# Optimization experiments

Hardware: AMD Instinct MI355X
Metric: run time of the kernel (lower is better)

## Reference

```python
import jax, jax.numpy as jnp
import numpy as np

HIDDEN = 2048
INTER = 1408
NUM_EXPERTS = 8
TOP_K = 2
BATCH, SEQ = 2, 1024


def setup_inputs() -> dict:
    key = jax.random.key(0)
    ks = jax.random.split(key, 8)
    s = 0.02
    return {
        "x": jax.random.normal(ks[0], (BATCH, SEQ, HIDDEN), dtype=jnp.float32),
        "router_w": jax.random.normal(ks[1], (NUM_EXPERTS, HIDDEN), dtype=jnp.float32) * s,
        "gate_w": jax.random.normal(ks[2], (NUM_EXPERTS, INTER, HIDDEN), dtype=jnp.float32) * s,
        "up_w": jax.random.normal(ks[3], (NUM_EXPERTS, INTER, HIDDEN), dtype=jnp.float32) * s,
        "down_w": jax.random.normal(ks[4], (NUM_EXPERTS, HIDDEN, INTER), dtype=jnp.float32) * s,
        "shared_gate_w": jax.random.normal(ks[5], (INTER, HIDDEN), dtype=jnp.float32) * s,
        "shared_up_w": jax.random.normal(ks[6], (INTER, HIDDEN), dtype=jnp.float32) * s,
        "shared_down_w": jax.random.normal(ks[7], (HIDDEN, INTER), dtype=jnp.float32) * s,
    }


def reference(x, router_w, gate_w, up_w, down_w,
              shared_gate_w, shared_up_w, shared_down_w):
    B, S, H = x.shape
    T = B * S
    E = router_w.shape[0]
    xf = x.reshape(T, H)

    # Router: softmax over experts, top-k selection, renormalized weights
    logits = xf @ router_w.T                       # [T, E]
    probs = jax.nn.softmax(logits, axis=-1)
    topw, topi = jax.lax.top_k(probs, TOP_K)       # [T, K]
    topw = topw / jnp.sum(topw, axis=-1, keepdims=True)

    # Combine weight per (token, expert): scatter-add of top-k weights
    comb = jnp.zeros((T, E), dtype=xf.dtype).at[
        jnp.arange(T)[:, None], topi].add(topw)    # [T, E]

    # All-expert SwiGLU (grouped GEMM form of masked gather/MLP/scatter)
    g = jnp.einsum('th,eih->tei', xf, gate_w)      # [T, E, I]
    u = jnp.einsum('th,eih->tei', xf, up_w)
    hmid = jax.nn.silu(g) * u
    eo = jnp.einsum('tei,ehi->teh', hmid, down_w)  # [T, E, H]
    out = jnp.einsum('te,teh->th', comb, eo)       # weighted combine

    # Shared expert applied to every token
    sh = (jax.nn.silu(xf @ shared_gate_w.T) * (xf @ shared_up_w.T)) @ shared_down_w.T
    out = out + sh
    return out.reshape(B, S, H)
```

## Files before the change

### kernel.cpp

```cpp
#include <hip/hip_runtime.h>
#include <cstdint>
#include <cstddef>

#define T_TOK 2048
#define HID   2048
#define INTER 1408
#define NEXP  8
#define NPAIR 6144
#define SLICE 2883584
#define BKS   32

typedef __bf16 bf16x8 __attribute__((ext_vector_type(8)));
typedef float  floatx4 __attribute__((ext_vector_type(4)));

static const size_t XB_OFF   = 0;
static const size_t HM_OFF   = XB_OFF + (size_t)T_TOK * HID * 2;
static const size_t GB_OFF   = HM_OFF + (size_t)NPAIR * INTER * 2;
static const size_t UB_OFF   = GB_OFF + (size_t)9 * SLICE * 2;
static const size_t DB_OFF   = UB_OFF + (size_t)9 * SLICE * 2;
static const size_t TOK_OFF  = DB_OFF + (size_t)9 * SLICE * 2;
static const size_t WGT_OFF  = TOK_OFF + (size_t)NPAIR * 4;
static const size_t TE_OFF   = WGT_OFF + (size_t)NPAIR * 4;
static const size_t TW_OFF   = TE_OFF + (size_t)T_TOK * 2 * 4;
static const size_t CTRL_OFF = TW_OFF + (size_t)T_TOK * 2 * 4;

static __device__ __forceinline__ unsigned short f2bf(float f) {
    unsigned u = __float_as_uint(f);
    u += 0x7fffu + ((u >> 16) & 1u);
    return (unsigned short)(u >> 16);
}
static __device__ __forceinline__ unsigned pk2(float a, float b) {
    return (unsigned)f2bf(a) | ((unsigned)f2bf(b) << 16);
}
static __device__ __forceinline__ void g2l16(const void* g, void* l) {
    __builtin_amdgcn_global_load_lds(
        (const __attribute__((address_space(1))) unsigned int*)g,
        (__attribute__((address_space(3))) unsigned int*)l, 16, 0, 0);
}

__global__ __launch_bounds__(256) void k_cvt_x(const float* __restrict__ x,
                                               unsigned short* __restrict__ xb) {
    int gid = blockIdx.x * 256 + threadIdx.x;
    const float4* src = (const float4*)x;
    float4 a = src[gid * 2], b = src[gid * 2 + 1];
    uint4 o;
    o.x = pk2(a.x, a.y); o.y = pk2(a.z, a.w);
    o.z = pk2(b.x, b.y); o.w = pk2(b.z, b.w);
    ((uint4*)xb)[gid] = o;
}

__global__ __launch_bounds__(256) void k_cvt_w(const float* __restrict__ g,
                                               const float* __restrict__ u,
                                               const float* __restrict__ d,
                                               const float* __restrict__ sg,
                                               const float* __restrict__ su,
                                               const float* __restrict__ sd,
                                               unsigned short* __restrict__ gb,
                                               unsigned short* __restrict__ ub,
                                               unsigned short* __restrict__ db) {
    int sl = blockIdx.z;
    const float* src;
    unsigned short* dst;
    if (blockIdx.y == 0) {
        src = (sl < 8) ? g + (size_t)sl * SLICE : sg;
        dst = gb + (size_t)sl * SLICE;
    } else if (blockIdx.y == 1) {
        src = (sl < 8) ? u + (size_t)sl * SLICE : su;
        dst = ub + (size_t)sl * SLICE;
    } else {
        src = (sl < 8) ? d + (size_t)sl * SLICE : sd;
        dst = db + (size_t)sl * SLICE;
    }
    int gid = blockIdx.x * 256 + threadIdx.x;
    const float4* s4 = (const float4*)src;
    float4 a = s4[gid * 2], b = s4[gid * 2 + 1];
    uint4 o;
    o.x = pk2(a.x, a.y); o.y = pk2(a.z, a.w);
    o.z = pk2(b.x, b.y); o.w = pk2(b.z, b.w);
    ((uint4*)dst)[gid] = o;
}

__global__ __launch_bounds__(256) void k_router(const float* __restrict__ x,
                                                const float* __restrict__ rw,
                                                int* __restrict__ te, float* __restrict__ tw,
                                                int* __restrict__ counts) {
    int wave = threadIdx.x >> 6, lane = threadIdx.x & 63;
    int t = blockIdx.x * 4 + wave;
    const float* xp = x + (size_t)t * HID;

    float acc[8];
#pragma unroll
    for (int e = 0; e < 8; ++e) acc[e] = 0.f;
    for (int i = lane; i < HID; i += 64) {
        float xv = xp[i];
#pragma unroll
        for (int e = 0; e < 8; ++e) acc[e] = fmaf(xv, rw[e * HID + i], acc[e]);
    }
#pragma unroll
    for (int e = 0; e < 8; ++e) {
        float v = acc[e];
        for (int s = 32; s; s >>= 1) v += __shfl_xor(v, s, 64);
        acc[e] = v;
    }
    float mx = acc[0];
#pragma unroll
    for (int e = 1; e < 8; ++e) mx = fmaxf(mx, acc[e]);
    float p[8];
#pragma unroll
    for (int e = 0; e < 8; ++e) p[e] = __expf(acc[e] - mx);
    int i1 = 0; float v1 = p[0];
#pragma unroll
    for (int e = 1; e < 8; ++e) if (p[e] > v1) { v1 = p[e]; i1 = e; }
    int i2 = -1; float v2 = -1.f;
#pragma unroll
    for (int e = 0; e < 8; ++e) if (e != i1 && p[e] > v2) { v2 = p[e]; i2 = e; }
    float inv = 1.f / (v1 + v2);
    if (lane == 0) {
        te[2 * t] = i1;     tw[2 * t] = v1 * inv;
        te[2 * t + 1] = i2; tw[2 * t + 1] = v2 * inv;
        atomicAdd(&counts[i1], 1);
        atomicAdd(&counts[i2], 1);
    }
}

__global__ void k_offsets(int* __restrict__ ctrl) {
    if (threadIdx.x == 0) {
        int s = 0;
        for (int e = 0; e < 8; ++e) { ctrl[16 + e] = s; s += ctrl[e]; }
        ctrl[16 + 8] = s;
        ctrl[8] = T_TOK;
    }
}

__global__ __launch_bounds__(256) void k_scatter(const int* __restrict__ te,
                                                 const float* __restrict__ tw,
                                                 const int* __restrict__ offsets,
                                                 int* __restrict__ fill,
                                                 int* __restrict__ tok, float* __restrict__ wgt) {
    int t = blockIdx.x * 256 + threadIdx.x;
    if (t >= T_TOK) return;
#pragma unroll
    for (int k = 0; k < 2; ++k) {
        int e = te[2 * t + k];
        int slot = atomicAdd(&fill[e], 1);
        int pp = offsets[e] + slot;
        tok[pp] = t; wgt[pp] = tw[2 * t + k];
    }
    tok[2 * T_TOK + t] = t; wgt[2 * T_TOK + t] = 1.0f;
}

__global__ __launch_bounds__(256) void k_gemm1(const unsigned short* __restrict__ xb,
                                               const unsigned short* __restrict__ gwb,
                                               const unsigned short* __restrict__ uwb,
                                               const int* __restrict__ tok,
                                               const int* __restrict__ ctrl,
                                               unsigned short* __restrict__ hmid) {
    int e = blockIdx.z;
    int cnt = ctrl[e];
    int m0 = blockIdx.y * 128;
    if (m0 >= cnt) return;
    int off = ctrl[16 + e];
    int i0 = blockIdx.x * 64;
    const unsigned short* gw = gwb + (size_t)e * SLICE;
    const unsigned short* uw = uwb + (size_t)e * SLICE;

    __shared__ __align__(16) unsigned short As[128 * BKS];
    __shared__ __align__(16) unsigned short Bg[64 * BKS];
    __shared__ __align__(16) unsigned short Bu[64 * BKS];

    int tid = threadIdx.x;
    int lane = tid & 63, wave = tid >> 6;
    int lr = lane >> 2, lc = (lane & 3) * 8;

    int r0 = m0 + wave * 32 + lr;
    int ap0 = off + r0;       if (ap0 > NPAIR - 1) ap0 = NPAIR - 1;
    int ap1 = off + r0 + 16;  if (ap1 > NPAIR - 1) ap1 = NPAIR - 1;
    const unsigned short* a0 = xb + (size_t)tok[ap0] * HID + lc;
    const unsigned short* a1 = xb + (size_t)tok[ap1] * HID + lc;
    const unsigned short* bg = gw + (size_t)(i0 + wave * 16 + lr) * HID + lc;
    const unsigned short* bu = uw + (size_t)(i0 + wave * 16 + lr) * HID + lc;

    unsigned short* lA0 = &As[(wave * 32) * BKS];
    unsigned short* lA1 = &As[(wave * 32 + 16) * BKS];
    unsigned short* lBg = &Bg[(wave * 16) * BKS];
    unsigned short* lBu = &Bu[(wave * 16) * BKS];

    floatx4 accg[2][4], accu[2][4];
#pragma unroll
    for (int mi = 0; mi < 2; ++mi)
#pragma unroll
        for (int ni = 0; ni < 4; ++ni) {
            accg[mi][ni] = (floatx4){0.f, 0.f, 0.f, 0.f};
            accu[mi][ni] = (floatx4){0.f, 0.f, 0.f, 0.f};
        }

    int wm = wave * 32;
    int mrow = lane & 15, kq = (lane >> 4) * 8;

    for (int kt = 0; kt < HID / BKS; ++kt) {
        int k0 = kt * BKS;
        g2l16(a0 + k0, lA0);
        g2l16(a1 + k0, lA1);
        g2l16(bg + k0, lBg);
        g2l16(bu + k0, lBu);
        __syncthreads();

        bf16x8 af[2];
#pragma unroll
        for (int mi = 0; mi < 2; ++mi)
            af[mi] = *(const bf16x8*)&As[(wm + mi * 16 + mrow) * BKS + kq];
#pragma unroll
        for (int ni = 0; ni < 4; ++ni) {
            bf16x8 bgv = *(const bf16x8*)&Bg[(ni * 16 + mrow) * BKS + kq];
            bf16x8 buv = *(const bf16x8*)&Bu[(ni * 16 + mrow) * BKS + kq];
#pragma unroll
            for (int mi = 0; mi < 2; ++mi) {
                accg[mi][ni] = __builtin_amdgcn_mfma_f32_16x16x32_bf16(af[mi], bgv, accg[mi][ni], 0, 0, 0);
                accu[mi][ni] = __builtin_amdgcn_mfma_f32_16x16x32_bf16(af[mi], buv, accu[mi][ni], 0, 0, 0);
            }
        }
        __syncthreads();
    }

    int quad = lane >> 4, col = lane & 15;
#pragma unroll
    for (int mi = 0; mi < 2; ++mi)
#pragma unroll
        for (int ni = 0; ni < 4; ++ni)
#pragma unroll
            for (int r = 0; r < 4; ++r) {
                int row = m0 + wm + mi * 16 + quad * 4 + r;
                if (row < cnt) {
                    float g = accg[mi][ni][r], u = accu[mi][ni][r];
                    float s = g / (1.f + __expf(-g));
                    hmid[(size_t)(off + row) * INTER + i0 + ni * 16 + col] = f2bf(s * u);
                }
            }
}

__global__ __launch_bounds__(256) void k_gemm2(const unsigned short* __restrict__ hmid,
                                               const unsigned short* __restrict__ dwb,
                                               const int* __restrict__ tok,
                                               const float* __restrict__ wgt,
                                               const int* __restrict__ ctrl,
                                               float* __restrict__ out) {
    int e = blockIdx.z;
    int cnt = ctrl[e];
    int m0 = blockIdx.y * 128;
    if (m0 >= cnt) return;
    int off = ctrl[16 + e];
    int n0 = blockIdx.x * 64;
    const unsigned short* dw = dwb + (size_t)e * SLICE;

    __shared__ __align__(16) unsigned short As[128 * BKS];
    __shared__ __align__(16) unsigned short Bd[64 * BKS];

    int tid = threadIdx.x;
    int lane = tid & 63, wave = tid >> 6;
    int lr = lane >> 2, lc = (lane & 3) * 8;

    int r0 = m0 + wave * 32 + lr;
    int ap0 = off + r0;       if (ap0 > NPAIR - 1) ap0 = NPAIR - 1;
    int ap1 = off + r0 + 16;  if (ap1 > NPAIR - 1) ap1 = NPAIR - 1;
    const unsigned short* a0 = hmid + (size_t)ap0 * INTER + lc;
    const unsigned short* a1 = hmid + (size_t)ap1 * INTER + lc;
    const unsigned short* bd = dw + (size_t)(n0 + wave * 16 + lr) * INTER + lc;

    unsigned short* lA0 = &As[(wave * 32) * BKS];
    unsigned short* lA1 = &As[(wave * 32 + 16) * BKS];
    unsigned short* lBd = &Bd[(wave * 16) * BKS];

    floatx4 acc[2][4];
#pragma unroll
    for (int mi = 0; mi < 2; ++mi)
#pragma unroll
        for (int ni = 0; ni < 4; ++ni) acc[mi][ni] = (floatx4){0.f, 0.f, 0.f, 0.f};

    int wm = wave * 32;
    int mrow = lane & 15, kq = (lane >> 4) * 8;

    for (int kt = 0; kt < INTER / BKS; ++kt) {
        int k0 = kt * BKS;
        g2l16(a0 + k0, lA0);
        g2l16(a1 + k0, lA1);
        g2l16(bd + k0, lBd);
        __syncthreads();

        bf16x8 af[2];
#pragma unroll
        for (int mi = 0; mi < 2; ++mi)
            af[mi] = *(const bf16x8*)&As[(wm + mi * 16 + mrow) * BKS + kq];
#pragma unroll
        for (int ni = 0; ni < 4; ++ni) {
            bf16x8 bv = *(const bf16x8*)&Bd[(ni * 16 + mrow) * BKS + kq];
#pragma unroll
            for (int mi = 0; mi < 2; ++mi)
                acc[mi][ni] = __builtin_amdgcn_mfma_f32_16x16x32_bf16(af[mi], bv, acc[mi][ni], 0, 0, 0);
        }
        __syncthreads();
    }

    int quad = lane >> 4, col = lane & 15;
#pragma unroll
    for (int mi = 0; mi < 2; ++mi)
#pragma unroll
        for (int r = 0; r < 4; ++r) {
            int row = m0 + wm + mi * 16 + quad * 4 + r;
            if (row < cnt) {
                int p = off + row;
                int t = tok[p];
                float w = wgt[p];
#pragma unroll
                for (int ni = 0; ni < 4; ++ni)
                    atomicAdd(&out[(size_t)t * HID + n0 + ni * 16 + col], w * acc[mi][ni][r]);
            }
        }
}

extern "C" void kernel_launch(void* const* d_in, const int* in_sizes, int n_in,
                              void* d_out, int out_size, void* d_ws, size_t ws_size,
                              hipStream_t stream) {
    const float* x        = (const float*)d_in[0];
    const float* router_w = (const float*)d_in[1];
    const float* gate_w   = (const float*)d_in[2];
    const float* up_w     = (const float*)d_in[3];
    const float* down_w   = (const float*)d_in[4];
    const float* sgate    = (const float*)d_in[5];
    const float* sup      = (const float*)d_in[6];
    const float* sdown    = (const float*)d_in[7];
    float* out = (float*)d_out;

    char* ws = (char*)d_ws;
    unsigned short* xb   = (unsigned short*)(ws + XB_OFF);
    unsigned short* hmid = (unsigned short*)(ws + HM_OFF);
    unsigned short* gwb  = (unsigned short*)(ws + GB_OFF);
    unsigned short* uwb  = (unsigned short*)(ws + UB_OFF);
    unsigned short* dwb  = (unsigned short*)(ws + DB_OFF);
    int*   tok  = (int*)(ws + TOK_OFF);
    float* wgt  = (float*)(ws + WGT_OFF);
    int*   te   = (int*)(ws + TE_OFF);
    float* tw   = (float*)(ws + TW_OFF);
    int*   ctrl = (int*)(ws + CTRL_OFF);

    hipMemsetAsync(ctrl, 0, 48 * sizeof(int), stream);
    hipMemsetAsync(out, 0, (size_t)T_TOK * HID * sizeof(float), stream);

    k_cvt_x  <<<(T_TOK * HID) / 8 / 256, 256, 0, stream>>>(x, xb);
    k_cvt_w  <<<dim3(SLICE / 8 / 256, 3, 9), 256, 0, stream>>>(gate_w, up_w, down_w,
                                                               sgate, sup, sdown, gwb, uwb, dwb);
    k_router <<<T_TOK / 4, 256, 0, stream>>>(x, router_w, te, tw, ctrl);
    k_offsets<<<1, 64, 0, stream>>>(ctrl);
    k_scatter<<<T_TOK / 256, 256, 0, stream>>>(te, tw, ctrl + 16, ctrl + 32, tok, wgt);

    k_gemm1<<<dim3(INTER / 64, 16, 9), 256, 0, stream>>>(xb, gwb, uwb, tok, ctrl, hmid);
    k_gemm2<<<dim3(HID / 64, 16, 9), 256, 0, stream>>>(hmid, dwb, tok, wgt, ctrl, out);
}
```

Baseline: 620.3 us.

## Double-buffer LDS in expert GEMMs, remap grid, fold offsets kernel into scatter

Both grouped GEMM kernels now ping-pong between two LDS buffers, so the global-to-LDS copy of the next K tile is issued while MFMAs run on the current one. This is meant to hide load latency. The 3D grid is flattened to 1D, and block indices are interleaved so that 8 consecutive blocks span different column tiles of the same M tile, which aims to improve L2 reuse of the A rows. The separate k_offsets launch is removed: expert offsets are recomputed from the counts inside the scatter and GEMM kernels. This saves a launch at the cost of a few redundant reads and twice the shared memory per block.

New measurement: 656.5 us. 1.06x slower.

```diff
diff --git a/kernel.cpp b/kernel.cpp
--- a/kernel.cpp
+++ b/kernel.cpp
@@ -9,6 +9,13 @@
 #define NPAIR 6144
 #define SLICE 2883584
 #define BKS   32
+
+#define NI1   22
+#define GP1   24
+#define NB1   (9 * GP1 * 16)
+#define NI2   32
+#define GP2   32
+#define NB2   (9 * GP2 * 16)
 
 typedef __bf16 bf16x8 __attribute__((ext_vector_type(8)));
 typedef float  floatx4 __attribute__((ext_vector_type(4)));
@@ -123,30 +130,76 @@
     }
 }
 
-__global__ void k_offsets(int* __restrict__ ctrl) {
-    if (threadIdx.x == 0) {
-        int s = 0;
-        for (int e = 0; e < 8; ++e) { ctrl[16 + e] = s; s += ctrl[e]; }
-        ctrl[16 + 8] = s;
-        ctrl[8] = T_TOK;
-    }
-}
-
 __global__ __launch_bounds__(256) void k_scatter(const int* __restrict__ te,
                                                  const float* __restrict__ tw,
-                                                 const int* __restrict__ offsets,
-                                                 int* __restrict__ fill,
+                                                 int* __restrict__ ctrl,
                                                  int* __restrict__ tok, float* __restrict__ wgt) {
+    __shared__ int soff[8];
+    if (threadIdx.x < 8) {
+        int s = 0;
+        for (int e = 0; e < (int)threadIdx.x; ++e) s += ctrl[e];
+        soff[threadIdx.x] = s;
+    }
+    __syncthreads();
     int t = blockIdx.x * 256 + threadIdx.x;
     if (t >= T_TOK) return;
 #pragma unroll
     for (int k = 0; k < 2; ++k) {
         int e = te[2 * t + k];
-        int slot = atomicAdd(&fill[e], 1);
-        int pp = offsets[e] + slot;
+        int slot = atomicAdd(&ctrl[8 + e], 1);
+        int pp = soff[e] + slot;
         tok[pp] = t; wgt[pp] = tw[2 * t + k];
     }
     tok[2 * T_TOK + t] = t; wgt[2 * T_TOK + t] = 1.0f;
+}
+
+__device__ __forceinline__ void stage4(const unsigned short* a0, const unsigned short* a1,
+                                       const unsigned short* b0, const unsigned short* b1, int k0,
+                                       unsigned short* lA0, unsigned short* lA1,
+                                       unsigned short* lB0, unsigned short* lB1) {
+    g2l16(a0 + k0, lA0);
+    g2l16(a1 + k0, lA1);
+    g2l16(b0 + k0, lB0);
+    g2l16(b1 + k0, lB1);
+}
+__device__ __forceinline__ void stage3(const unsigned short* a0, const unsigned short* a1,
+                                       const unsigned short* b0, int k0,
+                                       unsigned short* lA0, unsigned short* lA1,
+                                       unsigned short* lB0) {
+    g2l16(a0 + k0, lA0);
+    g2l16(a1 + k0, lA1);
+    g2l16(b0 + k0, lB0);
+}
+
+__device__ __forceinline__ void mfma_step1(const unsigned short* As,
+                                           const unsigned short* Bg,
+                                           const unsigned short* Bu,
+                                           int wm, int mrow, int kq,
+                                           floatx4 (&accg)[2][4], floatx4 (&accu)[2][4]) {
+    bf16x8 af0 = *(const bf16x8*)&As[(wm + mrow) * BKS + kq];
+    bf16x8 af1 = *(const bf16x8*)&As[(wm + 16 + mrow) * BKS + kq];
+#pragma unroll
+    for (int ni = 0; ni < 4; ++ni) {
+        bf16x8 bgv = *(const bf16x8*)&Bg[(ni * 16 + mrow) * BKS + kq];
+        bf16x8 buv = *(const bf16x8*)&Bu[(ni * 16 + mrow) * BKS + kq];
+        accg[0][ni] = __builtin_amdgcn_mfma_f32_16x16x32_bf16(af0, bgv, accg[0][ni], 0, 0, 0);
+        accu[0][ni] = __builtin_amdgcn_mfma_f32_16x16x32_bf16(af0, buv, accu[0][ni], 0, 0, 0);
+        accg[1][ni] = __builtin_amdgcn_mfma_f32_16x16x32_bf16(af1, bgv, accg[1][ni], 0, 0, 0);
+        accu[1][ni] = __builtin_amdgcn_mfma_f32_16x16x32_bf16(af1, buv, accu[1][ni], 0, 0, 0);
+    }
+}
+__device__ __forceinline__ void mfma_step2(const unsigned short* As,
+                                           const unsigned short* Bd,
+                                           int wm, int mrow, int kq,
+                                           floatx4 (&acc)[2][4]) {
+    bf16x8 af0 = *(const bf16x8*)&As[(wm + mrow) * BKS + kq];
+    bf16x8 af1 = *(const bf16x8*)&As[(wm + 16 + mrow) * BKS + kq];
+#pragma unroll
+    for (int ni = 0; ni < 4; ++ni) {
+        bf16x8 bv = *(const bf16x8*)&Bd[(ni * 16 + mrow) * BKS + kq];
+        acc[0][ni] = __builtin_amdgcn_mfma_f32_16x16x32_bf16(af0, bv, acc[0][ni], 0, 0, 0);
+        acc[1][ni] = __builtin_amdgcn_mfma_f32_16x16x32_bf16(af1, bv, acc[1][ni], 0, 0, 0);
+    }
 }
 
 __global__ __launch_bounds__(256) void k_gemm1(const unsigned short* __restrict__ xb,
@@ -155,18 +208,27 @@
                                                const int* __restrict__ tok,
                                                const int* __restrict__ ctrl,
                                                unsigned short* __restrict__ hmid) {
-    int e = blockIdx.z;
-    int cnt = ctrl[e];
-    int m0 = blockIdx.y * 128;
+    int h = blockIdx.x;
+    int g8  = h & 7;
+    int mt  = (h >> 3) & 15;
+    int j   = h >> 7;
+    int G   = j * 8 + g8;
+    int e   = G / GP1;
+    int bi  = G % GP1;
+    if (bi >= NI1) return;
+    int off = 0;
+#pragma unroll
+    for (int ee = 0; ee < 8; ++ee) if (ee < e) off += ctrl[ee];
+    int cnt = (e < 8) ? ctrl[e] : T_TOK;
+    int m0 = mt * 128;
     if (m0 >= cnt) return;
-    int off = ctrl[16 + e];
-    int i0 = blockIdx.x * 64;
+    int i0 = bi * 64;
     const unsigned short* gw = gwb + (size_t)e * SLICE;
     const unsigned short* uw = uwb + (size_t)e * SLICE;
 
-    __shared__ __align__(16) unsigned short As[128 * BKS];
-    __shared__ __align__(16) unsigned short Bg[64 * BKS];
-    __shared__ __align__(16) unsigned short Bu[64 * BKS];
+    __shared__ __align__(16) unsigned short As0[128 * BKS], As1[128 * BKS];
+    __shared__ __align__(16) unsigned short Bg0[64 * BKS],  Bg1[64 * BKS];
+    __shared__ __align__(16) unsigned short Bu0[64 * BKS],  Bu1[64 * BKS];
 
     int tid = threadIdx.x;
     int lane = tid & 63, wave = tid >> 6;
@@ -180,10 +242,7 @@
     const unsigned short* bg = gw + (size_t)(i0 + wave * 16 + lr) * HID + lc;
     const unsigned short* bu = uw + (size_t)(i0 + wave * 16 + lr) * HID + lc;
 
-    unsigned short* lA0 = &As[(wave * 32) * BKS];
-    unsigned short* lA1 = &As[(wave * 32 + 16) * BKS];
-    unsigned short* lBg = &Bg[(wave * 16) * BKS];
-    unsigned short* lBu = &Bu[(wave * 16) * BKS];
+    int wA0 = (wave * 32) * BKS, wA1 = (wave * 32 + 16) * BKS, wB = (wave * 16) * BKS;
 
     floatx4 accg[2][4], accu[2][4];
 #pragma unroll
@@ -197,28 +256,16 @@
     int wm = wave * 32;
     int mrow = lane & 15, kq = (lane >> 4) * 8;
 
-    for (int kt = 0; kt < HID / BKS; ++kt) {
-        int k0 = kt * BKS;
-        g2l16(a0 + k0, lA0);
-        g2l16(a1 + k0, lA1);
-        g2l16(bg + k0, lBg);
-        g2l16(bu + k0, lBu);
+    stage4(a0, a1, bg, bu, 0, &As0[wA0], &As0[wA1], &Bg0[wB], &Bu0[wB]);
+    __syncthreads();
+    const int NT = HID / BKS;
+    for (int kt = 0; kt < NT; kt += 2) {
+        stage4(a0, a1, bg, bu, (kt + 1) * BKS, &As1[wA0], &As1[wA1], &Bg1[wB], &Bu1[wB]);
+        mfma_step1(As0, Bg0, Bu0, wm, mrow, kq, accg, accu);
         __syncthreads();
-
-        bf16x8 af[2];
-#pragma unroll
-        for (int mi = 0; mi < 2; ++mi)
-            af[mi] = *(const bf16x8*)&As[(wm + mi * 16 + mrow) * BKS + kq];
-#pragma unroll
-        for (int ni = 0; ni < 4; ++ni) {
-            bf16x8 bgv = *(const bf16x8*)&Bg[(ni * 16 + mrow) * BKS + kq];
-            bf16x8 buv = *(const bf16x8*)&Bu[(ni * 16 + mrow) * BKS + kq];
-#pragma unroll
-            for (int mi = 0; mi < 2; ++mi) {
-                accg[mi][ni] = __builtin_amdgcn_mfma_f32_16x16x32_bf16(af[mi], bgv, accg[mi][ni], 0, 0, 0);
-                accu[mi][ni] = __builtin_amdgcn_mfma_f32_16x16x32_bf16(af[mi], buv, accu[mi][ni], 0, 0, 0);
-            }
-        }
+        if (kt + 2 < NT)
+            stage4(a0, a1, bg, bu, (kt + 2) * BKS, &As0[wA0], &As0[wA1], &Bg0[wB], &Bu0[wB]);
+        mfma_step1(As1, Bg1, Bu1, wm, mrow, kq, accg, accu);
         __syncthreads();
     }
 
@@ -244,16 +291,24 @@
                                                const float* __restrict__ wgt,
                                                const int* __restrict__ ctrl,
                                                float* __restrict__ out) {
-    int e = blockIdx.z;
-    int cnt = ctrl[e];
-    int m0 = blockIdx.y * 128;
+    int h = blockIdx.x;
+    int g8  = h & 7;
+    int mt  = (h >> 3) & 15;
+    int j   = h >> 7;
+    int G   = j * 8 + g8;
+    int e   = G / GP2;
+    int bn  = G % GP2;
+    int off = 0;
+#pragma unroll
+    for (int ee = 0; ee < 8; ++ee) if (ee < e) off += ctrl[ee];
+    int cnt = (e < 8) ? ctrl[e] : T_TOK;
+    int m0 = mt * 128;
     if (m0 >= cnt) return;
-    int off = ctrl[16 + e];
-    int n0 = blockIdx.x * 64;
+    int n0 = bn * 64;
     const unsigned short* dw = dwb + (size_t)e * SLICE;
 
-    __shared__ __align__(16) unsigned short As[128 * BKS];
-    __shared__ __align__(16) unsigned short Bd[64 * BKS];
+    __shared__ __align__(16) unsigned short As0[128 * BKS], As1[128 * BKS];
+    __shared__ __align__(16) unsigned short Bd0[64 * BKS],  Bd1[64 * BKS];
 
     int tid = threadIdx.x;
     int lane = tid & 63, wave = tid >> 6;
@@ -266,9 +321,7 @@
     const unsigned short* a1 = hmid + (size_t)ap1 * INTER + lc;
     const unsigned short* bd = dw + (size_t)(n0 + wave * 16 + lr) * INTER + lc;
 
-    unsigned short* lA0 = &As[(wave * 32) * BKS];
-    unsigned short* lA1 = &As[(wave * 32 + 16) * BKS];
-    unsigned short* lBd = &Bd[(wave * 16) * BKS];
+    int wA0 = (wave * 32) * BKS, wA1 = (wave * 32 + 16) * BKS, wB = (wave * 16) * BKS;
 
     floatx4 acc[2][4];
 #pragma unroll
@@ -279,24 +332,16 @@
     int wm = wave * 32;
     int mrow = lane & 15, kq = (lane >> 4) * 8;
 
-    for (int kt = 0; kt < INTER / BKS; ++kt) {
-        int k0 = kt * BKS;
-        g2l16(a0 + k0, lA0);
-        g2l16(a1 + k0, lA1);
-        g2l16(bd + k0, lBd);
+    stage3(a0, a1, bd, 0, &As0[wA0], &As0[wA1], &Bd0[wB]);
+    __syncthreads();
+    const int NT = INTER / BKS;
+    for (int kt = 0; kt < NT; kt += 2) {
+        stage3(a0, a1, bd, (kt + 1) * BKS, &As1[wA0], &As1[wA1], &Bd1[wB]);
+        mfma_step2(As0, Bd0, wm, mrow, kq, acc);
         __syncthreads();
-
-        bf16x8 af[2];
-#pragma unroll
-        for (int mi = 0; mi < 2; ++mi)
-            af[mi] = *(const bf16x8*)&As[(wm + mi * 16 + mrow) * BKS + kq];
-#pragma unroll
-        for (int ni = 0; ni < 4; ++ni) {
-            bf16x8 bv = *(const bf16x8*)&Bd[(ni * 16 + mrow) * BKS + kq];
-#pragma unroll
-            for (int mi = 0; mi < 2; ++mi)
-                acc[mi][ni] = __builtin_amdgcn_mfma_f32_16x16x32_bf16(af[mi], bv, acc[mi][ni], 0, 0, 0);
-        }
+        if (kt + 2 < NT)
+            stage3(a0, a1, bd, (kt + 2) * BKS, &As0[wA0], &As0[wA1], &Bd0[wB]);
+        mfma_step2(As1, Bd1, wm, mrow, kq, acc);
         __syncthreads();
     }
 
@@ -342,16 +387,15 @@
     float* tw   = (float*)(ws + TW_OFF);
     int*   ctrl = (int*)(ws + CTRL_OFF);
 
-    hipMemsetAsync(ctrl, 0, 48 * sizeof(int), stream);
+    hipMemsetAsync(ctrl, 0, 16 * sizeof(int), stream);
     hipMemsetAsync(out, 0, (size_t)T_TOK * HID * sizeof(float), stream);
 
     k_cvt_x  <<<(T_TOK * HID) / 8 / 256, 256, 0, stream>>>(x, xb);
     k_cvt_w  <<<dim3(SLICE / 8 / 256, 3, 9), 256, 0, stream>>>(gate_w, up_w, down_w,
                                                                sgate, sup, sdown, gwb, uwb, dwb);
     k_router <<<T_TOK / 4, 256, 0, stream>>>(x, router_w, te, tw, ctrl);
-    k_offsets<<<1, 64, 0, stream>>>(ctrl);
-    k_scatter<<<T_TOK / 256, 256, 0, stream>>>(te, tw, ctrl + 16, ctrl + 32, tok, wgt);
-
-    k_gemm1<<<dim3(INTER / 64, 16, 9), 256, 0, stream>>>(xb, gwb, uwb, tok, ctrl, hmid);
-    k_gemm2<<<dim3(HID / 64, 16, 9), 256, 0, stream>>>(hmid, dwb, tok, wgt, ctrl, out);
-}
+    k_scatter<<<T_TOK / 256, 256, 0, stream>>>(te, tw, ctrl, tok, wgt);
+
+    k_gemm1<<<NB1, 256, 0, stream>>>(xb, gwb, uwb, tok, ctrl, hmid);
+    k_gemm2<<<NB2, 256, 0, stream>>>(hmid, dwb, tok, wgt, ctrl, out);
+}
```
